# Optimization experiments

Measured on AMD Instinct MI355X. Metric: run time of the kernel, lower is better.

Reference implementation:

```python
import jax, jax.numpy as jnp
import numpy as np

N_NODES = 100000
N_EDGES = 600000
IN_DIM, HID, OUT = 6, 128, 1
EPS = 1e-5


def _glorot(key, shape):
    fan_in, fan_out = shape[1], shape[0]
    lim = jnp.sqrt(6.0 / (fan_in + fan_out))
    return jax.random.uniform(key, shape, jnp.float32, -lim, lim)


def setup_inputs() -> dict:
    key = jax.random.key(0)
    ks = jax.random.split(key, 16)
    x = jax.random.normal(ks[0], (N_NODES, IN_DIM), jnp.float32)
    edge_index = jax.random.randint(ks[1], (2, N_EDGES), 0, N_NODES, jnp.int64)
    return {
        "x": x,
        "edge_index": edge_index,
        # SAGEConv layer 0: 6 -> 128 (lin_l acts on aggregated neighbors, lin_r on root)
        "w_l0": _glorot(ks[2], (HID, IN_DIM)), "b_l0": jnp.zeros((HID,), jnp.float32),
        "w_r0": _glorot(ks[3], (HID, IN_DIM)),
        "bn_g0": jnp.ones((HID,), jnp.float32), "bn_b0": jnp.zeros((HID,), jnp.float32),
        # SAGEConv layer 1: 128 -> 128
        "w_l1": _glorot(ks[4], (HID, HID)), "b_l1": jnp.zeros((HID,), jnp.float32),
        "w_r1": _glorot(ks[5], (HID, HID)),
        "bn_g1": jnp.ones((HID,), jnp.float32), "bn_b1": jnp.zeros((HID,), jnp.float32),
        # SAGEConv layer 2: 128 -> 1
        "w_l2": _glorot(ks[6], (OUT, HID)), "b_l2": jnp.zeros((OUT,), jnp.float32),
        "w_r2": _glorot(ks[7], (OUT, HID)),
    }


def _sage_conv(x, src, dst, inv_deg, w_l, b_l, w_r):
    # mean aggregation of source-node features into destination nodes
    agg = jax.ops.segment_sum(x[src], dst, num_segments=N_NODES)  # [N, d]
    mean_nb = agg * inv_deg[:, None]
    return mean_nb @ w_l.T + b_l + x @ w_r.T


def _batch_norm(x, gamma, beta):
    mu = jnp.mean(x, axis=0)
    var = jnp.mean(jnp.square(x - mu), axis=0)  # biased, as torch BN training
    return (x - mu) * jax.lax.rsqrt(var + EPS) * gamma + beta


def reference(x, edge_index, w_l0, b_l0, w_r0, bn_g0, bn_b0,
              w_l1, b_l1, w_r1, bn_g1, bn_b1, w_l2, b_l2, w_r2):
    src, dst = edge_index[0], edge_index[1]
    deg = jax.ops.segment_sum(jnp.ones_like(dst, dtype=x.dtype), dst,
                              num_segments=N_NODES)
    inv_deg = 1.0 / jnp.maximum(deg, 1.0)

    h = _sage_conv(x, src, dst, inv_deg, w_l0, b_l0, w_r0)
    h = jax.nn.relu(_batch_norm(h, bn_g0, bn_b0))  # dropout = identity (eval)

    h = _sage_conv(h, src, dst, inv_deg, w_l1, b_l1, w_r1)
    h = jax.nn.relu(_batch_norm(h, bn_g1, bn_b1))

    h = _sage_conv(h, src, dst, inv_deg, w_l2, b_l2, w_r2)
    return jax.nn.sigmoid(h).squeeze(-1)  # [N]
```

## Files before the change

kernel.cpp:

```cpp
#include <hip/hip_runtime.h>
#include <math.h>

#define HID 128
#define INDIM 6

typedef float4 f4;
typedef __attribute__((ext_vector_type(8))) short short8;
typedef __attribute__((ext_vector_type(4))) float f32x4;

static __device__ inline unsigned short f2bf(float f) {
    union { float f; unsigned int u; } v; v.f = f;
    unsigned int r = v.u + 0x7fffu + ((v.u >> 16) & 1u);
    return (unsigned short)(r >> 16);
}
static __device__ inline float bf2f_lo(unsigned int u) {
    union { unsigned int u; float f; } v; v.u = u << 16; return v.f;
}
static __device__ inline float bf2f_hi(unsigned int u) {
    union { unsigned int u; float f; } v; v.u = u & 0xffff0000u; return v.f;
}

__global__ void k_zero2(int* a, int na, int* b, int nb) {
    int i = blockIdx.x * blockDim.x + threadIdx.x;
    if (i < na) a[i] = 0;
    if (i < nb) b[i] = 0;
}

__global__ void k_deg(const int* dst, int* deg, int* rank, int E) {
    int e = blockIdx.x * blockDim.x + threadIdx.x;
    if (e < E) rank[e] = atomicAdd(&deg[dst[e]], 1);
}

__global__ void k_scan_partial(const int* __restrict__ deg, int* __restrict__ partial, int N) {
    __shared__ int lds[256];
    int t = threadIdx.x;
    int base = blockIdx.x * 1024 + t * 4;
    int s = 0;
    if (base + 4 <= N) {
        int4 v = *(const int4*)&deg[base];
        s = v.x + v.y + v.z + v.w;
    } else {
        for (int i = 0; i < 4; i++) if (base + i < N) s += deg[base + i];
    }
    lds[t] = s;
    __syncthreads();
    for (int off = 128; off > 0; off >>= 1) {
        if (t < off) lds[t] += lds[t + off];
        __syncthreads();
    }
    if (t == 0) partial[blockIdx.x] = lds[0];
}

__global__ void k_scan_tops(int* partial, int nb) {
    __shared__ int lds[1024];
    int t = threadIdx.x;
    lds[t] = (t < nb) ? partial[t] : 0;
    __syncthreads();
    for (int off = 1; off < 1024; off <<= 1) {
        int v = (t >= off) ? lds[t - off] : 0;
        __syncthreads();
        lds[t] += v;
        __syncthreads();
    }
    if (t < nb) partial[t] = (t == 0) ? 0 : lds[t - 1];
}

__global__ void k_scan_write(const int* __restrict__ deg, const int* __restrict__ partial,
                             int* __restrict__ rowptr, int N, int E) {
    __shared__ int lds[256];
    int t = threadIdx.x;
    int base = blockIdx.x * 1024 + t * 4;
    int v0 = 0, v1 = 0, v2 = 0, v3 = 0;
    if (base + 4 <= N) {
        int4 v = *(const int4*)&deg[base];
        v0 = v.x; v1 = v.y; v2 = v.z; v3 = v.w;
    } else {
        if (base + 0 < N) v0 = deg[base + 0];
        if (base + 1 < N) v1 = deg[base + 1];
        if (base + 2 < N) v2 = deg[base + 2];
        if (base + 3 < N) v3 = deg[base + 3];
    }
    lds[t] = v0 + v1 + v2 + v3;
    __syncthreads();
    for (int off = 1; off < 256; off <<= 1) {
        int v = (t >= off) ? lds[t - off] : 0;
        __syncthreads();
        lds[t] += v;
        __syncthreads();
    }
    int run = partial[blockIdx.x] + ((t == 0) ? 0 : lds[t - 1]);
    if (base + 0 < N) rowptr[base + 0] = run; run += v0;
    if (base + 1 < N) rowptr[base + 1] = run; run += v1;
    if (base + 2 < N) rowptr[base + 2] = run; run += v2;
    if (base + 3 < N) rowptr[base + 3] = run; run += v3;
    if (blockIdx.x == 0 && t == 0) rowptr[N] = E;
}

__global__ void k_fill(const int* ei, const int* rank, const int* rowptr, int* csr, int E) {
    int e = blockIdx.x * blockDim.x + threadIdx.x;
    if (e < E) {
        int d = ei[E + e];
        csr[rowptr[d] + rank[e]] = ei[e];
    }
}

__global__ void k_invdeg(const int* deg, float* invd, int N) {
    int i = blockIdx.x * blockDim.x + threadIdx.x;
    if (i < N) invd[i] = 1.0f / (float)max(deg[i], 1);
}

__global__ void k_prepw(const float* __restrict__ wl, const float* __restrict__ wr,
                        unsigned short* __restrict__ wcat) {
    int i = blockIdx.x * 256 + threadIdx.x;
    int o = i >> 8, k = i & 255;
    float v = (k < 128) ? wl[o * 128 + k] : wr[o * 128 + k - 128];
    wcat[i] = f2bf(v);
}

__global__ __launch_bounds__(256) void k_l0stats(
        const float* __restrict__ x, const int* __restrict__ rowptr,
        const int* __restrict__ csr, const float* __restrict__ invd,
        const float* __restrict__ wl, const float* __restrict__ bl,
        const float* __restrict__ wr, float* __restrict__ mean6,
        float* __restrict__ sum8, float* __restrict__ sq8, int N) {
    __shared__ float wlds[1600];
    __shared__ float blds[136];
    __shared__ float mx[32][8];
    __shared__ float xr[32][8];
    __shared__ float ps[4][128];
    __shared__ float pq[4][128];
    int t = threadIdx.x;
    for (int idx = t; idx < 1536; idx += 256) {
        int half = idx >= 768 ? 1 : 0;
        int lin = idx - half * 768;
        int o = lin / 6, i = lin - o * 6;
        float v = half ? wr[lin] : wl[lin];
        wlds[half * 800 + o * 6 + i + (o >> 4) * 2] = v;
    }
    if (t < 128) blds[t + (t >> 4)] = bl[t];
    int nl = t >> 3, f = t & 7;
    int n = blockIdx.x * 32 + nl;
    bool valid = n < N;
    if (f < 6) {
        float mean = 0.f, xv = 0.f;
        if (valid) {
            int s = rowptr[n], e = rowptr[n + 1];
            float acc = 0.f;
            int i = s;
            for (; i + 4 <= e; i += 4) {
                int i0 = csr[i], i1 = csr[i + 1], i2 = csr[i + 2], i3 = csr[i + 3];
                float a0 = x[i0 * 6 + f], a1 = x[i1 * 6 + f];
                float a2 = x[i2 * 6 + f], a3 = x[i3 * 6 + f];
                acc += (a0 + a1) + (a2 + a3);
            }
            for (; i < e; i++) acc += x[csr[i] * 6 + f];
            mean = acc * invd[n];
            xv = x[n * 6 + f];
            mean6[n * 6 + f] = mean;
        }
        mx[nl][f] = mean;
        xr[nl][f] = xv;
    }
    __syncthreads();
    float m0 = mx[nl][0], m1 = mx[nl][1], m2 = mx[nl][2];
    float m3 = mx[nl][3], m4 = mx[nl][4], m5 = mx[nl][5];
    float r0 = xr[nl][0], r1 = xr[nl][1], r2 = xr[nl][2];
    float r3 = xr[nl][3], r4 = xr[nl][4], r5 = xr[nl][5];
    const float* wA = wlds;
    const float* wB = wlds + 800;
    int wv = t >> 6, lane = t & 63;
#pragma unroll
    for (int k = 0; k < 16; k++) {
        int o = f * 16 + k;
        int wb = 98 * f + 6 * k;
        float h = blds[o + f];
        h += m0 * wA[wb] + m1 * wA[wb + 1] + m2 * wA[wb + 2]
           + m3 * wA[wb + 3] + m4 * wA[wb + 4] + m5 * wA[wb + 5];
        h += r0 * wB[wb] + r1 * wB[wb + 1] + r2 * wB[wb + 2]
           + r3 * wB[wb + 3] + r4 * wB[wb + 4] + r5 * wB[wb + 5];
        float s = valid ? h : 0.f;
        float q = s * s;
        s += __shfl_xor(s, 8, 64);  q += __shfl_xor(q, 8, 64);
        s += __shfl_xor(s, 16, 64); q += __shfl_xor(q, 16, 64);
        s += __shfl_xor(s, 32, 64); q += __shfl_xor(q, 32, 64);
        if (lane < 8) { ps[wv][lane * 16 + k] = s; pq[wv][lane * 16 + k] = q; }
    }
    __syncthreads();
    if (t < 128) {
        float S = ps[0][t] + ps[1][t] + ps[2][t] + ps[3][t];
        float Q = pq[0][t] + pq[1][t] + pq[2][t] + pq[3][t];
        int slot = (blockIdx.x & 7) * 128 + t;
        atomicAdd(&sum8[slot], S);
        atomicAdd(&sq8[slot], Q);
    }
}

__global__ __launch_bounds__(256) void k_l0apply(
        const float* __restrict__ x, const float* __restrict__ mean6,
        const float* __restrict__ wl, const float* __restrict__ bl,
        const float* __restrict__ wr, const float* __restrict__ scale,
        const float* __restrict__ shift, unsigned short* __restrict__ out, int N) {
    __shared__ float wlds[1600];
    __shared__ float blds[136];
    __shared__ float sclds[136];
    __shared__ float shlds[136];
    __shared__ float mx[32][8];
    __shared__ float xr[32][8];
    int t = threadIdx.x;
    for (int idx = t; idx < 1536; idx += 256) {
        int half = idx >= 768 ? 1 : 0;
        int lin = idx - half * 768;
        int o = lin / 6, i = lin - o * 6;
        float v = half ? wr[lin] : wl[lin];
        wlds[half * 800 + o * 6 + i + (o >> 4) * 2] = v;
    }
    if (t < 128) {
        blds[t + (t >> 4)]  = bl[t];
        sclds[t + (t >> 4)] = scale[t];
        shlds[t + (t >> 4)] = shift[t];
    }
    int nl = t >> 3, f = t & 7;
    int n = blockIdx.x * 32 + nl;
    bool valid = n < N;
    if (f < 6) {
        mx[nl][f] = valid ? mean6[n * 6 + f] : 0.f;
        xr[nl][f] = valid ? x[n * 6 + f] : 0.f;
    }
    __syncthreads();
    if (!valid) return;
    float m0 = mx[nl][0], m1 = mx[nl][1], m2 = mx[nl][2];
    float m3 = mx[nl][3], m4 = mx[nl][4], m5 = mx[nl][5];
    float r0 = xr[nl][0], r1 = xr[nl][1], r2 = xr[nl][2];
    float r3 = xr[nl][3], r4 = xr[nl][4], r5 = xr[nl][5];
    const float* wA = wlds;
    const float* wB = wlds + 800;
    unsigned short pk[16];
#pragma unroll
    for (int k4 = 0; k4 < 4; k4++) {
#pragma unroll
        for (int j = 0; j < 4; j++) {
            int k = k4 * 4 + j;
            int o = f * 16 + k;
            int wb = 98 * f + 6 * k;
            float h = blds[o + f];
            h += m0 * wA[wb] + m1 * wA[wb + 1] + m2 * wA[wb + 2]
               + m3 * wA[wb + 3] + m4 * wA[wb + 4] + m5 * wA[wb + 5];
            h += r0 * wB[wb] + r1 * wB[wb + 1] + r2 * wB[wb + 2]
               + r3 * wB[wb + 3] + r4 * wB[wb + 4] + r5 * wB[wb + 5];
            pk[k] = f2bf(fmaxf(0.f, fmaf(h, sclds[o + f], shlds[o + f])));
        }
    }
    unsigned short* dst = out + (size_t)n * HID + f * 16;
    *(uint4*)(dst)     = *(const uint4*)&pk[0];
    *(uint4*)(dst + 8) = *(const uint4*)&pk[8];
}

__global__ void k_bnfin8(const float* sum8, const float* sq8, const float* g, const float* b,
                         float* scale, float* shift, float invN) {
    int t = threadIdx.x;
    float s = 0.f, q = 0.f;
    for (int c = 0; c < 8; c++) { s += sum8[c * 128 + t]; q += sq8[c * 128 + t]; }
    float mu  = s * invN;
    float var = q * invN - mu * mu;
    float sc  = g[t] * rsqrtf(var + 1e-5f);
    scale[t] = sc;
    shift[t] = b[t] - mu * sc;
}

__global__ void k_agg_bf(const unsigned short* __restrict__ hb, const int* __restrict__ rowptr,
                         const int* __restrict__ csr, const float* __restrict__ invd,
                         unsigned short* __restrict__ out, int N) {
    int t = threadIdx.x;
    int w = t >> 6, lid = t & 63;
    int half = lid >> 5, l32 = lid & 31;
    int n = blockIdx.x * 8 + w * 2 + half;
    if (n >= N) return;
    int s = rowptr[n], e = rowptr[n + 1];
    const uint2* hb64 = (const uint2*)hb;
    float ax0 = 0.f, ay0 = 0.f, ax1 = 0.f, ay1 = 0.f;
    int i = s;
    for (; i + 4 <= e; i += 4) {
        int i0 = csr[i], i1 = csr[i + 1], i2 = csr[i + 2], i3 = csr[i + 3];
        uint2 u0 = hb64[(size_t)i0 * 32 + l32];
        uint2 u1 = hb64[(size_t)i1 * 32 + l32];
        uint2 u2 = hb64[(size_t)i2 * 32 + l32];
        uint2 u3 = hb64[(size_t)i3 * 32 + l32];
        ax0 += (bf2f_lo(u0.x) + bf2f_lo(u1.x)) + (bf2f_lo(u2.x) + bf2f_lo(u3.x));
        ay0 += (bf2f_hi(u0.x) + bf2f_hi(u1.x)) + (bf2f_hi(u2.x) + bf2f_hi(u3.x));
        ax1 += (bf2f_lo(u0.y) + bf2f_lo(u1.y)) + (bf2f_lo(u2.y) + bf2f_lo(u3.y));
        ay1 += (bf2f_hi(u0.y) + bf2f_hi(u1.y)) + (bf2f_hi(u2.y) + bf2f_hi(u3.y));
    }
    for (; i < e; i++) {
        uint2 u = hb64[(size_t)csr[i] * 32 + l32];
        ax0 += bf2f_lo(u.x); ay0 += bf2f_hi(u.x);
        ax1 += bf2f_lo(u.y); ay1 += bf2f_hi(u.y);
    }
    float id = invd[n];
    uint2 r;
    r.x = (unsigned int)f2bf(ax0 * id) | ((unsigned int)f2bf(ay0 * id) << 16);
    r.y = (unsigned int)f2bf(ax1 * id) | ((unsigned int)f2bf(ay1 * id) << 16);
    ((uint2*)out)[(size_t)n * 32 + l32] = r;
}

__global__ __launch_bounds__(256) void k_gemm(
        const unsigned short* __restrict__ Bm, const unsigned short* __restrict__ Ar,
        const unsigned short* __restrict__ wcat, const float* __restrict__ bias,
        float* __restrict__ sum8, float* __restrict__ sq8,
        unsigned short* __restrict__ C, int N) {
    __shared__ __align__(16) unsigned short As[128][72];
    __shared__ float lds_s[2][128];
    __shared__ float lds_q[2][128];
    int t = threadIdx.x;
    int wave = t >> 6, lane = t & 63;
    int wr = wave >> 1, wc = wave & 1;
    int row0 = blockIdx.x * 128;
    int r = t >> 1, half = t & 1;
    int lrow = lane & 15, koff = (lane >> 4) * 8;

    f32x4 acc[4][4];
#pragma unroll
    for (int m = 0; m < 4; m++)
#pragma unroll
        for (int n = 0; n < 4; n++) acc[m][n] = (f32x4)(0.f);

    for (int chunk = 0; chunk < 4; chunk++) {
        int kb = chunk * 64;
        int srow = row0 + r;
        int c0 = (kb & 127) + half * 32;
        const unsigned short* src = (kb < 128) ? Bm : Ar;
        uint4 v0, v1, v2, v3;
        if (srow < N) {
            const unsigned short* p = src + (size_t)srow * HID + c0;
            v0 = *(const uint4*)(p);      v1 = *(const uint4*)(p + 8);
            v2 = *(const uint4*)(p + 16); v3 = *(const uint4*)(p + 24);
        } else {
            v0 = v1 = v2 = v3 = make_uint4(0, 0, 0, 0);
        }
        *(uint4*)&As[r][half * 32]      = v0;
        *(uint4*)&As[r][half * 32 + 8]  = v1;
        *(uint4*)&As[r][half * 32 + 16] = v2;
        *(uint4*)&As[r][half * 32 + 24] = v3;
        __syncthreads();

#pragma unroll
        for (int ks = 0; ks < 64; ks += 32) {
            short8 af[4], bfr[4];
#pragma unroll
            for (int m = 0; m < 4; m++)
                af[m] = *(const short8*)&As[wr * 64 + m * 16 + lrow][ks + koff];
#pragma unroll
            for (int n = 0; n < 4; n++)
                bfr[n] = *(const short8*)&wcat[(size_t)(wc * 64 + n * 16 + lrow) * 256 + kb + ks + koff];
#pragma unroll
            for (int m = 0; m < 4; m++)
#pragma unroll
                for (int n = 0; n < 4; n++)
                    acc[m][n] = __builtin_amdgcn_mfma_f32_16x16x32_bf16(af[m], bfr[n], acc[m][n], 0, 0, 0);
        }
        __syncthreads();
    }

    int cl = lane & 15, rq = (lane >> 4) * 4;
    float cs[4], cq[4];
#pragma unroll
    for (int n = 0; n < 4; n++) {
        int col = wc * 64 + n * 16 + cl;
        float bn = bias[col];
        float s = 0.f, q = 0.f;
#pragma unroll
        for (int m = 0; m < 4; m++) {
#pragma unroll
            for (int reg = 0; reg < 4; reg++) {
                int row = row0 + wr * 64 + m * 16 + rq + reg;
                float v = acc[m][n][reg] + bn;
                if (row < N) {
                    C[(size_t)row * HID + col] = f2bf(v);
                    s += v;
                    q += v * v;
                }
            }
        }
        cs[n] = s; cq[n] = q;
    }
#pragma unroll
    for (int n = 0; n < 4; n++) {
        float s = cs[n], q = cq[n];
        s += __shfl_xor(s, 16, 64); q += __shfl_xor(q, 16, 64);
        s += __shfl_xor(s, 32, 64); q += __shfl_xor(q, 32, 64);
        if (lane < 16) {
            int col = wc * 64 + n * 16 + cl;
            lds_s[wr][col] = s;
            lds_q[wr][col] = q;
        }
    }
    __syncthreads();
    if (t < 128) {
        float S = lds_s[0][t] + lds_s[1][t];
        float Q = lds_q[0][t] + lds_q[1][t];
        int slot = (blockIdx.x & 7) * 128 + t;
        atomicAdd(&sum8[slot], S);
        atomicAdd(&sq8[slot], Q);
    }
}

__global__ void k_dots(const unsigned short* __restrict__ h, const float* __restrict__ scale,
                       const float* __restrict__ shift, const float* __restrict__ wl2,
                       const float* __restrict__ wr2, float* __restrict__ s_arr,
                       float* __restrict__ r_arr, int N) {
    int w = threadIdx.x >> 6, lid = threadIdx.x & 63;
    int n = blockIdx.x * 4 + w;
    if (n >= N) return;
    unsigned int u = ((const unsigned int*)h)[(size_t)n * 64 + lid];
    float hx = bf2f_lo(u), hy = bf2f_hi(u);
    float2 sc = *(const float2*)&scale[lid * 2];
    float2 sh = *(const float2*)&shift[lid * 2];
    float y0 = fmaxf(0.f, fmaf(hx, sc.x, sh.x));
    float y1 = fmaxf(0.f, fmaf(hy, sc.y, sh.y));
    float2 wl = *(const float2*)&wl2[lid * 2];
    float2 wrv = *(const float2*)&wr2[lid * 2];
    float ps = y0 * wl.x + y1 * wl.y;
    float pr = y0 * wrv.x + y1 * wrv.y;
#pragma unroll
    for (int off = 32; off > 0; off >>= 1) {
        ps += __shfl_down(ps, off, 64);
        pr += __shfl_down(pr, off, 64);
    }
    if (lid == 0) { s_arr[n] = ps; r_arr[n] = pr; }
}

__global__ void k_final2(const float* __restrict__ s_arr, const float* __restrict__ r_arr,
                         const int* __restrict__ rowptr, const int* __restrict__ csr,
                         const float* __restrict__ invd, const float* __restrict__ bl2,
                         float* __restrict__ out, int N) {
    int n = blockIdx.x * blockDim.x + threadIdx.x;
    if (n >= N) return;
    int s = rowptr[n], e = rowptr[n + 1];
    float a = 0.f;
    int i = s;
    for (; i + 4 <= e; i += 4) {
        float a0 = s_arr[csr[i]],     a1 = s_arr[csr[i + 1]];
        float a2 = s_arr[csr[i + 2]], a3 = s_arr[csr[i + 3]];
        a += (a0 + a1) + (a2 + a3);
    }
    for (; i < e; i++) a += s_arr[csr[i]];
    float p = a * invd[n] + r_arr[n] + bl2[0];
    out[n] = 1.f / (1.f + expf(-p));
}

extern "C" void kernel_launch(void* const* d_in, const int* in_sizes, int n_in,
                              void* d_out, int out_size, void* d_ws, size_t ws_size,
                              hipStream_t stream) {
    const float* x   = (const float*)d_in[0];
    const int*   ei  = (const int*)d_in[1];
    const float* wl0 = (const float*)d_in[2];
    const float* bl0 = (const float*)d_in[3];
    const float* wr0 = (const float*)d_in[4];
    const float* g0  = (const float*)d_in[5];
    const float* be0 = (const float*)d_in[6];
    const float* wl1 = (const float*)d_in[7];
    const float* bl1 = (const float*)d_in[8];
    const float* wr1 = (const float*)d_in[9];
    const float* g1  = (const float*)d_in[10];
    const float* be1 = (const float*)d_in[11];
    const float* wl2 = (const float*)d_in[12];
    const float* bl2 = (const float*)d_in[13];
    const float* wr2 = (const float*)d_in[14];
    float* outp = (float*)d_out;

    int N = in_sizes[0] / INDIM;
    int E = in_sizes[1] / 2;

    char* ws = (char*)d_ws;
    size_t off = 0;
    auto alloc = [&](size_t bytes) { size_t o = off; off = (off + bytes + 255) & ~(size_t)255; return o; };
    int*   degi   = (int*)(ws + alloc((size_t)N * 4));
    int*   rank   = (int*)(ws + alloc((size_t)E * 4));
    int*   rowptr = (int*)(ws + alloc((size_t)(N + 1) * 4));
    int*   csr    = (int*)(ws + alloc((size_t)E * 4));
    float* invd   = (float*)(ws + alloc((size_t)N * 4));
    int*   partial= (int*)(ws + alloc(1024 * 4));
    float* bnbuf  = (float*)(ws + alloc(5120 * 4));
    unsigned short* wcat = (unsigned short*)(ws + alloc(128 * 256 * 2));
    float* sarr   = (float*)(ws + alloc((size_t)N * 4));
    float* rarr   = (float*)(ws + alloc((size_t)N * 4));
    float* mean6  = (float*)(ws + alloc((size_t)N * 6 * 4));
    float* sum0_8 = bnbuf;
    float* sq0_8  = bnbuf + 1024;
    float* sum1_8 = bnbuf + 2048;
    float* sq1_8  = bnbuf + 3072;
    float* sc0 = bnbuf + 4096, *sh0 = bnbuf + 4224;
    float* sc1 = bnbuf + 4352, *sh1 = bnbuf + 4480;
    unsigned short* bufB = (unsigned short*)(ws + alloc((size_t)N * HID * 2));
    unsigned short* bufC = (unsigned short*)(ws + alloc((size_t)N * HID * 2));
    unsigned short* bufD = (unsigned short*)(ws + alloc((size_t)N * HID * 2));

    float invN = 1.0f / (float)N;
    int gE = (E + 255) / 256;
    int gN = (N + 255) / 256;
    int gW = (N + 3) / 4;
    int gA = (N + 7) / 8;
    int gL = (N + 31) / 32;
    int gS = (N + 127) / 128;
    int nbScan = (N + 1023) / 1024;

    k_zero2<<<gN, 256, 0, stream>>>(degi, N, (int*)bnbuf, 4096);

    k_prepw<<<128, 256, 0, stream>>>(wl1, wr1, wcat);

    k_deg<<<gE, 256, 0, stream>>>(ei + E, degi, rank, E);
    k_scan_partial<<<nbScan, 256, 0, stream>>>(degi, partial, N);
    k_scan_tops<<<1, 1024, 0, stream>>>(partial, nbScan);
    k_scan_write<<<nbScan, 256, 0, stream>>>(degi, partial, rowptr, N, E);
    k_fill<<<gE, 256, 0, stream>>>(ei, rank, rowptr, csr, E);
    k_invdeg<<<gN, 256, 0, stream>>>(degi, invd, N);

    k_l0stats<<<gL, 256, 0, stream>>>(x, rowptr, csr, invd, wl0, bl0, wr0, mean6,
                                      sum0_8, sq0_8, N);
    k_bnfin8<<<1, 128, 0, stream>>>(sum0_8, sq0_8, g0, be0, sc0, sh0, invN);

    k_l0apply<<<gL, 256, 0, stream>>>(x, mean6, wl0, bl0, wr0, sc0, sh0, bufC, N);

    k_agg_bf<<<gA, 256, 0, stream>>>(bufC, rowptr, csr, invd, bufD, N);
    k_gemm<<<gS, 256, 0, stream>>>(bufD, bufC, wcat, bl1, sum1_8, sq1_8, bufB, N);
    k_bnfin8<<<1, 128, 0, stream>>>(sum1_8, sq1_8, g1, be1, sc1, sh1, invN);

    k_dots<<<gW, 256, 0, stream>>>(bufB, sc1, sh1, wl2, wr2, sarr, rarr, N);
    k_final2<<<gN, 256, 0, stream>>>(sarr, rarr, rowptr, csr, invd, bl2, outp, N);
}
```

Measured before the change: 214.8 us.

## Stage GEMM weights and output tile through LDS for coalesced access

Weight fragments are now copied once per K-chunk into a shared-memory tile, so each wave no longer reads them straight from global memory. The output tile is first written into the reused A-tile buffer with padding, then stored as coalesced 16-byte row segments instead of scattered 2-byte stores. The goal is to cut uncoalesced global traffic in the GEMM epilogue and redundant weight loads. The cost is more LDS, which may lower occupancy. The output staging writes 128x136 elements into a buffer declared as 128x72, so it silently relies on the weight buffer being placed directly after it.

```diff
diff --git a/kernel.cpp b/kernel.cpp
--- a/kernel.cpp
+++ b/kernel.cpp
@@ -308,6 +308,7 @@
         float* __restrict__ sum8, float* __restrict__ sq8,
         unsigned short* __restrict__ C, int N) {
     __shared__ __align__(16) unsigned short As[128][72];
+    __shared__ __align__(16) unsigned short Ws[128][72];
     __shared__ float lds_s[2][128];
     __shared__ float lds_q[2][128];
     int t = threadIdx.x;
@@ -328,18 +329,23 @@
         int srow = row0 + r;
         int c0 = (kb & 127) + half * 32;
         const unsigned short* src = (kb < 128) ? Bm : Ar;
-        uint4 v0, v1, v2, v3;
+        uint4 a0, a1, a2, a3;
         if (srow < N) {
             const unsigned short* p = src + (size_t)srow * HID + c0;
-            v0 = *(const uint4*)(p);      v1 = *(const uint4*)(p + 8);
-            v2 = *(const uint4*)(p + 16); v3 = *(const uint4*)(p + 24);
+            a0 = *(const uint4*)(p);      a1 = *(const uint4*)(p + 8);
+            a2 = *(const uint4*)(p + 16); a3 = *(const uint4*)(p + 24);
         } else {
-            v0 = v1 = v2 = v3 = make_uint4(0, 0, 0, 0);
+            a0 = a1 = a2 = a3 = make_uint4(0, 0, 0, 0);
         }
-        *(uint4*)&As[r][half * 32]      = v0;
-        *(uint4*)&As[r][half * 32 + 8]  = v1;
-        *(uint4*)&As[r][half * 32 + 16] = v2;
-        *(uint4*)&As[r][half * 32 + 24] = v3;
+        *(uint4*)&As[r][half * 32]      = a0;
+        *(uint4*)&As[r][half * 32 + 8]  = a1;
+        *(uint4*)&As[r][half * 32 + 16] = a2;
+        *(uint4*)&As[r][half * 32 + 24] = a3;
+        const unsigned short* wp = wcat + r * 256 + kb + half * 32;
+        *(uint4*)&Ws[r][half * 32]      = *(const uint4*)(wp);
+        *(uint4*)&Ws[r][half * 32 + 8]  = *(const uint4*)(wp + 8);
+        *(uint4*)&Ws[r][half * 32 + 16] = *(const uint4*)(wp + 16);
+        *(uint4*)&Ws[r][half * 32 + 24] = *(const uint4*)(wp + 24);
         __syncthreads();
 
 #pragma unroll
@@ -350,7 +356,7 @@
                 af[m] = *(const short8*)&As[wr * 64 + m * 16 + lrow][ks + koff];
 #pragma unroll
             for (int n = 0; n < 4; n++)
-                bfr[n] = *(const short8*)&wcat[(size_t)(wc * 64 + n * 16 + lrow) * 256 + kb + ks + koff];
+                bfr[n] = *(const short8*)&Ws[wc * 64 + n * 16 + lrow][ks + koff];
 #pragma unroll
             for (int m = 0; m < 4; m++)
 #pragma unroll
@@ -360,6 +366,7 @@
         __syncthreads();
     }
 
+    unsigned short* Cst = &As[0][0];
     int cl = lane & 15, rq = (lane >> 4) * 4;
     float cs[4], cq[4];
 #pragma unroll
@@ -371,13 +378,10 @@
         for (int m = 0; m < 4; m++) {
 #pragma unroll
             for (int reg = 0; reg < 4; reg++) {
-                int row = row0 + wr * 64 + m * 16 + rq + reg;
+                int rl = wr * 64 + m * 16 + rq + reg;
                 float v = acc[m][n][reg] + bn;
-                if (row < N) {
-                    C[(size_t)row * HID + col] = f2bf(v);
-                    s += v;
-                    q += v * v;
-                }
+                Cst[rl * 136 + col] = f2bf(v);
+                if (row0 + rl < N) { s += v; q += v * v; }
             }
         }
         cs[n] = s; cq[n] = q;
@@ -400,6 +404,14 @@
         int slot = (blockIdx.x & 7) * 128 + t;
         atomicAdd(&sum8[slot], S);
         atomicAdd(&sq8[slot], Q);
+    }
+#pragma unroll
+    for (int j = 0; j < 8; j++) {
+        int idx = t + j * 256;
+        int rl = idx >> 4, seg = idx & 15;
+        int row = row0 + rl;
+        if (row < N)
+            *(uint4*)(C + (size_t)row * HID + seg * 8) = *(const uint4*)&Cst[rl * 136 + seg * 8];
     }
 }
 
```

New measurement: 193.1 us. 10.1% less time.
